# Optimization experiments

Measured on AMD Instinct MI355X. Metric: run time of the kernel, lower is better.

Reference implementation:

```python
import jax, jax.numpy as jnp
import numpy as np

N = 50000      # num_nodes
E = 800000     # num_edges (avg degree 16)
IC, OC = 2, 2  # in_channels, out_channels
DIN, DOUT = 128, 128
K = 3          # number of hops


def setup_inputs() -> dict:
    key = jax.random.key(0)
    k1, k2, k3, k4 = jax.random.split(key, 4)
    x = jax.random.normal(k1, (IC, N, DIN), dtype=jnp.float32)
    edge_index = jax.random.randint(k2, (2, E), 0, N, dtype=jnp.int32)
    a = np.sqrt(6.0 / (DIN + DOUT)).astype(np.float32)  # xavier_uniform bound
    W = jax.random.uniform(k3, (OC, IC, DIN, DOUT), minval=-a, maxval=a, dtype=jnp.float32)
    params = jax.random.uniform(k4, (OC, IC, K + 1), minval=0.0, maxval=0.01, dtype=jnp.float32)
    return {"x": x, "edge_index": edge_index, "W": W, "params": params}


def reference(x, edge_index, W, params):
    # x: [IC, N, DIN]; edge_index: [2, E]; W: [OC, IC, DIN, DOUT]; params: [OC, IC, K+1]
    n = x.shape[1]
    k_hops = params.shape[-1] - 1
    row, col = edge_index[0], edge_index[1]

    # normalize_adj: symmetric D^-1/2 A D^-1/2 on unit-valued edges
    deg = jax.ops.segment_sum(jnp.ones(row.shape[0], x.dtype), row, num_segments=n)
    dinv = jnp.where(deg > 0, jax.lax.rsqrt(deg), jnp.zeros_like(deg))
    val = dinv[row] * dinv[col]  # [E]

    def spmm(X):  # A_norm @ X per channel; X: [IC, N, d]
        gathered = X[:, col, :] * val[None, :, None]  # [IC, E, d]
        return jax.vmap(lambda g: jax.ops.segment_sum(g, row, num_segments=n))(gathered)

    # Hop features: H[m] = A^m x, computed once (hoisting the redundant spmm in the torch loop)
    hops = [x]
    for _ in range(k_hops):
        hops.append(spmm(hops[-1]))
    H = jnp.stack(hops)  # [K+1, IC, N, DIN]

    # out[i] = sum_j sum_m params[i,j,m] * (A^m x_j) @ W[i,j]
    return jnp.einsum('mjnd,ijm,ijdf->inf', H, params, W)  # [OC, N, DOUT]
```

## Files before the change

kernel.cpp:

```cpp
#include <hip/hip_runtime.h>
#include <hip/hip_bf16.h>
#include <stdint.h>

#define NN 50000
#define NE 800000
#define D 128
#define KH 3
#define SCAN_B ((NN + 255) / 256)

typedef __attribute__((ext_vector_type(8))) __bf16 bf16x8;
typedef __attribute__((ext_vector_type(4))) float f32x4;

__device__ __forceinline__ uint16_t bf16_rne(float f) {
  uint32_t u = __builtin_bit_cast(uint32_t, f);
  u = (u + 0x7fffu + ((u >> 16) & 1u)) >> 16;
  return (uint16_t)u;
}

#define GLDS16(gp, lp)                                                         \
  __builtin_amdgcn_global_load_lds(                                            \
      (__attribute__((address_space(1))) void*)(gp),                           \
      (__attribute__((address_space(3))) void*)(lp), 16, 0, 0)

__global__ void k_deg(const int* __restrict__ row, int* __restrict__ deg) {
  int e = blockIdx.x * 256 + threadIdx.x;
  if (e < NE) atomicAdd(&deg[row[e]], 1);
}

__global__ void k_dinv_bsum(const int* __restrict__ deg, float* __restrict__ dinv,
                            int* __restrict__ bsum) {
  __shared__ int s[256];
  int t = threadIdx.x;
  int i = blockIdx.x * 256 + t;
  int d = (i < NN) ? deg[i] : 0;
  if (i < NN) dinv[i] = (d > 0) ? rsqrtf((float)d) : 0.0f;
  s[t] = d;
  __syncthreads();
  for (int off = 128; off > 0; off >>= 1) {
    if (t < off) s[t] += s[t + off];
    __syncthreads();
  }
  if (t == 0) bsum[blockIdx.x] = s[0];
}

__global__ void k_bscan(const int* __restrict__ bsum, int* __restrict__ boff) {
  __shared__ int s[256];
  int t = threadIdx.x;
  int v = (t < SCAN_B) ? bsum[t] : 0;
  s[t] = v;
  __syncthreads();
  for (int off = 1; off < 256; off <<= 1) {
    int u = (t >= off) ? s[t - off] : 0;
    __syncthreads();
    s[t] += u;
    __syncthreads();
  }
  boff[t] = s[t] - v;
}

__global__ void k_rpwrite(const int* __restrict__ deg, const int* __restrict__ boff,
                          int* __restrict__ rp, int* __restrict__ cur) {
  __shared__ int s[256];
  int t = threadIdx.x;
  int i = blockIdx.x * 256 + t;
  int v = (i < NN) ? deg[i] : 0;
  s[t] = v;
  __syncthreads();
  for (int off = 1; off < 256; off <<= 1) {
    int u = (t >= off) ? s[t - off] : 0;
    __syncthreads();
    s[t] += u;
    __syncthreads();
  }
  if (i < NN) {
    int r = boff[blockIdx.x] + s[t] - v;
    rp[i] = r;
    cur[i] = r;
  }
  if (i == 0) rp[NN] = NE;
}

__global__ void k_scatter(const int* __restrict__ row, const int* __restrict__ col,
                          const float* __restrict__ dinv, int* __restrict__ cur,
                          int2* __restrict__ csr) {
  int e = blockIdx.x * 256 + threadIdx.x;
  if (e < NE) {
    int r = row[e], c = col[e];
    int pos = atomicAdd(&cur[r], 1);
    csr[pos] = make_int2(c, __float_as_int(dinv[r] * dinv[c]));
  }
}

__global__ void k_prep_c(const float* __restrict__ x, const float* __restrict__ W,
                         const float* __restrict__ params, uint16_t* __restrict__ dst,
                         uint16_t* __restrict__ wb) {
  int b = blockIdx.x, t = threadIdx.x;
  if (b < NN) {
    int idx = b * 256 + t;
    int n = idx >> 8, c = idx & 255, j = c >> 7, dd = c & 127;
    dst[idx] = bf16_rne(x[(size_t)j * NN * D + (size_t)n * D + dd]);
  } else {
    int idx = (b - NN) * 256 + t;
    int c = idx >> 10, k = idx & 1023;
    int i = c >> 7, f = c & 127, m = k >> 8, j = (k >> 7) & 1, dd = k & 127;
    float p = params[(i * 2 + j) * 4 + m];
    float w = W[((i * 2 + j) * 128 + dd) * 128 + f];
    wb[idx] = bf16_rne(p * w);
  }
}

__global__ void k_wbig_f(const float* __restrict__ W, const float* __restrict__ params,
                         uint16_t* __restrict__ wb) {
  int idx = blockIdx.x * 256 + threadIdx.x;
  if (idx >= 2 * 256 * 512) return;
  int j = idx >> 17, c = (idx >> 9) & 255, k = idx & 511;
  int i = c >> 7, f = c & 127, m = k >> 7, dd = k & 127;
  float p = params[(i * 2 + j) * 4 + m];
  float w = W[((i * 2 + j) * 128 + dd) * 128 + f];
  wb[idx] = bf16_rne(p * w);
}

__global__ void k_x2h_f(const float* __restrict__ xj, uint16_t* __restrict__ dst) {
  int idx = blockIdx.x * 256 + threadIdx.x;
  if (idx < NN * D) dst[idx] = bf16_rne(xj[idx]);
}

template <int NCH>
__global__ void k_spmm(const int* __restrict__ rp, const int2* __restrict__ csr,
                       const uint16_t* __restrict__ src, uint16_t* __restrict__ dst) {
  constexpr int STRIDE = NCH * 128;
  typedef uint32_t gvec __attribute__((ext_vector_type(NCH)));
  const int lane = threadIdx.x & 63;
  const int wid = threadIdx.x >> 6;
  const int r = blockIdx.x * 4 + wid;
  if (r >= NN) return;
  const int s = __builtin_amdgcn_readfirstlane(rp[r]);
  const int e = __builtin_amdgcn_readfirstlane(rp[r + 1]);
  const int lo = lane * 2 * NCH;

  float a[2 * NCH] = {};
  int i = s;
  for (; i + 8 <= e; i += 8) {
    int2 cv[8];
    gvec g[8];
#pragma unroll
    for (int u = 0; u < 8; ++u) cv[u] = csr[i + u];
#pragma unroll
    for (int u = 0; u < 8; ++u)
      g[u] = *(const gvec*)(src + (size_t)cv[u].x * STRIDE + lo);
#pragma unroll
    for (int u = 0; u < 8; ++u) {
      float v = __int_as_float(cv[u].y);
#pragma unroll
      for (int q = 0; q < NCH; ++q) {
        a[2 * q] = fmaf(v, __builtin_bit_cast(float, g[u][q] << 16), a[2 * q]);
        a[2 * q + 1] =
            fmaf(v, __builtin_bit_cast(float, g[u][q] & 0xffff0000u), a[2 * q + 1]);
      }
    }
  }
  for (; i + 4 <= e; i += 4) {
    int2 cv[4];
    gvec g[4];
#pragma unroll
    for (int u = 0; u < 4; ++u) cv[u] = csr[i + u];
#pragma unroll
    for (int u = 0; u < 4; ++u)
      g[u] = *(const gvec*)(src + (size_t)cv[u].x * STRIDE + lo);
#pragma unroll
    for (int u = 0; u < 4; ++u) {
      float v = __int_as_float(cv[u].y);
#pragma unroll
      for (int q = 0; q < NCH; ++q) {
        a[2 * q] = fmaf(v, __builtin_bit_cast(float, g[u][q] << 16), a[2 * q]);
        a[2 * q + 1] =
            fmaf(v, __builtin_bit_cast(float, g[u][q] & 0xffff0000u), a[2 * q + 1]);
      }
    }
  }
  for (; i < e; ++i) {
    int2 cv = csr[i];
    float v = __int_as_float(cv.y);
    gvec g = *(const gvec*)(src + (size_t)cv.x * STRIDE + lo);
#pragma unroll
    for (int q = 0; q < NCH; ++q) {
      a[2 * q] = fmaf(v, __builtin_bit_cast(float, g[q] << 16), a[2 * q]);
      a[2 * q + 1] = fmaf(v, __builtin_bit_cast(float, g[q] & 0xffff0000u), a[2 * q + 1]);
    }
  }
  gvec o;
#pragma unroll
  for (int q = 0; q < NCH; ++q)
    o[q] = ((uint32_t)bf16_rne(a[2 * q + 1]) << 16) | (uint32_t)bf16_rne(a[2 * q]);
  *(gvec*)(dst + (size_t)r * STRIDE + lo) = o;
}

template <int KTOT, int HOPW, int ACCUM>
__global__ __launch_bounds__(256) void k_gemm(
    const uint16_t* __restrict__ h0, const uint16_t* __restrict__ h1,
    const uint16_t* __restrict__ h2, const uint16_t* __restrict__ h3,
    const uint16_t* __restrict__ wb, float* __restrict__ out) {
  __shared__ __align__(16) uint16_t As[128 * 32];
  __shared__ __align__(16) uint16_t Bs[128 * 32];
  const uint16_t* hops[4] = {h0, h1, h2, h3};
  int t = threadIdx.x;
  int lane = t & 63, wid = t >> 6;
  int wm = wid >> 1, wn = wid & 1;
  int m0 = blockIdx.x * 128;
  int c0 = blockIdx.y * 128;
  int rl = lane & 15, q = lane >> 4;
  f32x4 acc[4][4] = {};
#pragma unroll
  for (int hop = 0; hop < KTOT / HOPW; ++hop) {
    const uint16_t* hm = hops[hop];
    for (int kin = 0; kin < HOPW; kin += 32) {
      int k0 = hop * HOPW + kin;
#pragma unroll
      for (int rr = 0; rr < 2; ++rr) {
        int c = rr * 256 + t;
        int row = c >> 2, kcL = c & 3;
        int kcG = kcL ^ (row & 3);
        int gr = m0 + row;
        gr = gr < NN ? gr : NN - 1;
        GLDS16(hm + (size_t)gr * HOPW + kin + kcG * 8, &As[c * 8]);
      }
#pragma unroll
      for (int rr = 0; rr < 2; ++rr) {
        int c = rr * 256 + t;
        int cc = c >> 2, kcL = c & 3;
        int kcG = kcL ^ (cc & 3);
        GLDS16(wb + (size_t)(c0 + cc) * KTOT + k0 + kcG * 8, &Bs[c * 8]);
      }
      __syncthreads();
      bf16x8 af[4], bq[4];
#pragma unroll
      for (int f = 0; f < 4; ++f) {
        int row = wm * 64 + f * 16 + rl;
        int kc = q ^ (rl & 3);
        af[f] = *(const bf16x8*)(&As[row * 32 + kc * 8]);
      }
#pragma unroll
      for (int f = 0; f < 4; ++f) {
        int row = wn * 64 + f * 16 + rl;
        int kc = q ^ (rl & 3);
        bq[f] = *(const bf16x8*)(&Bs[row * 32 + kc * 8]);
      }
#pragma unroll
      for (int fm = 0; fm < 4; ++fm)
#pragma unroll
        for (int fn = 0; fn < 4; ++fn)
          acc[fm][fn] = __builtin_amdgcn_mfma_f32_16x16x32_bf16(af[fm], bq[fn],
                                                                acc[fm][fn], 0, 0, 0);
      __syncthreads();
    }
  }
  int iOut = blockIdx.y;
#pragma unroll
  for (int fm = 0; fm < 4; ++fm) {
#pragma unroll
    for (int r = 0; r < 4; ++r) {
      int rowg = m0 + wm * 64 + fm * 16 + q * 4 + r;
      if (rowg >= NN) continue;
      float* op = out + ((size_t)iOut * NN + rowg) * D;
#pragma unroll
      for (int fn = 0; fn < 4; ++fn) {
        int colg = wn * 64 + fn * 16 + rl;
        if (ACCUM)
          op[colg] += acc[fm][fn][r];
        else
          op[colg] = acc[fm][fn][r];
      }
    }
  }
}

extern "C" void kernel_launch(void* const* d_in, const int* in_sizes, int n_in,
                              void* d_out, int out_size, void* d_ws, size_t ws_size,
                              hipStream_t stream) {
  (void)in_sizes; (void)n_in; (void)out_size;
  const float* x = (const float*)d_in[0];
  const int* ei = (const int*)d_in[1];
  const float* W = (const float*)d_in[2];
  const float* params = (const float*)d_in[3];
  float* out = (float*)d_out;
  char* ws = (char*)d_ws;

  size_t off = 0;
  auto take = [&](size_t bytes) {
    char* p = ws + off;
    off = (off + bytes + 255) & ~(size_t)255;
    return p;
  };
  int* deg = (int*)take((size_t)NN * 4);
  float* dinv = (float*)take((size_t)NN * 4);
  int* rp = (int*)take((size_t)(NN + 1) * 4);
  int* cur = (int*)take((size_t)NN * 4);
  int* bsum = (int*)take(256 * 4);
  int* boff = (int*)take(256 * 4);
  int2* csr = (int2*)take((size_t)NE * 8);
  uint16_t* wb = (uint16_t*)take((size_t)256 * 1024 * 2);
  size_t fixed = off;

  hipMemsetAsync(deg, 0, (size_t)NN * 4, stream);
  k_deg<<<(NE + 255) / 256, 256, 0, stream>>>(ei, deg);
  k_dinv_bsum<<<SCAN_B, 256, 0, stream>>>(deg, dinv, bsum);
  k_bscan<<<1, 256, 0, stream>>>(bsum, boff);
  k_rpwrite<<<SCAN_B, 256, 0, stream>>>(deg, boff, rp, cur);
  k_scatter<<<(NE + 255) / 256, 256, 0, stream>>>(ei, ei + NE, dinv, cur, csr);

  size_t hopC = (size_t)NN * 256 * 2;
  size_t needC = fixed + 4 * hopC + 1024;

  if (ws_size >= needC) {
    uint16_t* hop[4];
    for (int m = 0; m < 4; ++m) hop[m] = (uint16_t*)take(hopC);
    k_prep_c<<<NN + 1024, 256, 0, stream>>>(x, W, params, hop[0], wb);
    for (int m = 1; m <= KH; ++m)
      k_spmm<2><<<(NN + 3) / 4, 256, 0, stream>>>(rp, csr, hop[m - 1], hop[m]);
    dim3 grid((NN + 127) / 128, 2);
    k_gemm<1024, 256, 0><<<grid, 256, 0, stream>>>(hop[0], hop[1], hop[2], hop[3],
                                                   wb, out);
  } else {
    size_t hopF = (size_t)NN * 128 * 2;
    uint16_t* hop[4];
    for (int m = 0; m < 4; ++m) hop[m] = (uint16_t*)take(hopF);
    k_wbig_f<<<(2 * 256 * 512 + 255) / 256, 256, 0, stream>>>(W, params, wb);
    for (int j = 0; j < 2; ++j) {
      k_x2h_f<<<(NN * D + 255) / 256, 256, 0, stream>>>(x + (size_t)j * NN * D, hop[0]);
      for (int m = 1; m <= KH; ++m)
        k_spmm<1><<<(NN + 3) / 4, 256, 0, stream>>>(rp, csr, hop[m - 1], hop[m]);
      dim3 grid((NN + 127) / 128, 2);
      if (j == 0)
        k_gemm<512, 128, 0><<<grid, 256, 0, stream>>>(hop[0], hop[1], hop[2], hop[3],
                                                      wb, out);
      else
        k_gemm<512, 128, 1><<<grid, 256, 0, stream>>>(hop[0], hop[1], hop[2], hop[3],
                                                      wb + 256 * 512, out);
    }
  }
}
```

Before: 417.0 us.

## Fuse block scan into rpwrite, vectorize prep, split-wave SpMM, K=64 GEMM tiles

Removes the separate block-offset scan kernel by having each rpwrite block reduce the preceding block sums itself. Vectorizes the x-to-bf16 conversion to 8 elements per thread. Restructures SpMM so each half-wave handles alternate edges with wider 16-byte gathers, then combines the halves with a cross-lane shuffle. Doubles the GEMM K tile to 64 with an 8-way XOR swizzle, which halves the number of barriers but doubles LDS use per block.

```diff
diff --git a/kernel.cpp b/kernel.cpp
--- a/kernel.cpp
+++ b/kernel.cpp
@@ -15,6 +15,9 @@
   uint32_t u = __builtin_bit_cast(uint32_t, f);
   u = (u + 0x7fffu + ((u >> 16) & 1u)) >> 16;
   return (uint16_t)u;
+}
+__device__ __forceinline__ uint32_t bf16_pack(float lo, float hi) {
+  return ((uint32_t)bf16_rne(hi) << 16) | (uint32_t)bf16_rne(lo);
 }
 
 #define GLDS16(gp, lp)                                                         \
@@ -43,26 +46,22 @@
   if (t == 0) bsum[blockIdx.x] = s[0];
 }
 
-__global__ void k_bscan(const int* __restrict__ bsum, int* __restrict__ boff) {
-  __shared__ int s[256];
-  int t = threadIdx.x;
-  int v = (t < SCAN_B) ? bsum[t] : 0;
-  s[t] = v;
-  __syncthreads();
-  for (int off = 1; off < 256; off <<= 1) {
-    int u = (t >= off) ? s[t - off] : 0;
-    __syncthreads();
-    s[t] += u;
-    __syncthreads();
-  }
-  boff[t] = s[t] - v;
-}
-
-__global__ void k_rpwrite(const int* __restrict__ deg, const int* __restrict__ boff,
+__global__ void k_rpwrite(const int* __restrict__ deg, const int* __restrict__ bsum,
                           int* __restrict__ rp, int* __restrict__ cur) {
   __shared__ int s[256];
+  __shared__ int sboff;
   int t = threadIdx.x;
-  int i = blockIdx.x * 256 + t;
+  int b = blockIdx.x;
+  int pv = (t < b) ? bsum[t] : 0;
+  s[t] = pv;
+  __syncthreads();
+  for (int off = 128; off > 0; off >>= 1) {
+    if (t < off) s[t] += s[t + off];
+    __syncthreads();
+  }
+  if (t == 0) sboff = s[0];
+  __syncthreads();
+  int i = b * 256 + t;
   int v = (i < NN) ? deg[i] : 0;
   s[t] = v;
   __syncthreads();
@@ -73,7 +72,7 @@
     __syncthreads();
   }
   if (i < NN) {
-    int r = boff[blockIdx.x] + s[t] - v;
+    int r = sboff + s[t] - v;
     rp[i] = r;
     cur[i] = r;
   }
@@ -91,16 +90,26 @@
   }
 }
 
+#define XB 6250
 __global__ void k_prep_c(const float* __restrict__ x, const float* __restrict__ W,
                          const float* __restrict__ params, uint16_t* __restrict__ dst,
                          uint16_t* __restrict__ wb) {
   int b = blockIdx.x, t = threadIdx.x;
-  if (b < NN) {
-    int idx = b * 256 + t;
-    int n = idx >> 8, c = idx & 255, j = c >> 7, dd = c & 127;
-    dst[idx] = bf16_rne(x[(size_t)j * NN * D + (size_t)n * D + dd]);
+  if (b < XB) {
+    int base = (b * 256 + t) * 8;
+    int n = base >> 8, c0 = base & 255;
+    int j = c0 >> 7, dd = c0 & 127;
+    const float* xp = x + (size_t)j * NN * D + (size_t)n * D + dd;
+    float4 f0 = *(const float4*)xp;
+    float4 f1 = *(const float4*)(xp + 4);
+    uint4 o;
+    o.x = bf16_pack(f0.x, f0.y);
+    o.y = bf16_pack(f0.z, f0.w);
+    o.z = bf16_pack(f1.x, f1.y);
+    o.w = bf16_pack(f1.z, f1.w);
+    *(uint4*)(dst + base) = o;
   } else {
-    int idx = (b - NN) * 256 + t;
+    int idx = (b - XB) * 256 + t;
     int c = idx >> 10, k = idx & 1023;
     int i = c >> 7, f = c & 127, m = k >> 8, j = (k >> 7) & 1, dd = k & 127;
     float p = params[(i * 2 + j) * 4 + m];
@@ -129,22 +138,24 @@
 __global__ void k_spmm(const int* __restrict__ rp, const int2* __restrict__ csr,
                        const uint16_t* __restrict__ src, uint16_t* __restrict__ dst) {
   constexpr int STRIDE = NCH * 128;
-  typedef uint32_t gvec __attribute__((ext_vector_type(NCH)));
+  constexpr int NDW = NCH * 2;
+  typedef uint32_t gvec __attribute__((ext_vector_type(NDW)));
   const int lane = threadIdx.x & 63;
   const int wid = threadIdx.x >> 6;
   const int r = blockIdx.x * 4 + wid;
   if (r >= NN) return;
   const int s = __builtin_amdgcn_readfirstlane(rp[r]);
   const int e = __builtin_amdgcn_readfirstlane(rp[r + 1]);
-  const int lo = lane * 2 * NCH;
-
-  float a[2 * NCH] = {};
+  const int half = lane >> 5;
+  const int lo = (lane & 31) * 2 * NDW;
+
+  float a[2 * NDW] = {};
   int i = s;
-  for (; i + 8 <= e; i += 8) {
+  for (; i + 16 <= e; i += 16) {
     int2 cv[8];
     gvec g[8];
 #pragma unroll
-    for (int u = 0; u < 8; ++u) cv[u] = csr[i + u];
+    for (int u = 0; u < 8; ++u) cv[u] = csr[i + 2 * u + half];
 #pragma unroll
     for (int u = 0; u < 8; ++u)
       g[u] = *(const gvec*)(src + (size_t)cv[u].x * STRIDE + lo);
@@ -152,47 +163,41 @@
     for (int u = 0; u < 8; ++u) {
       float v = __int_as_float(cv[u].y);
 #pragma unroll
-      for (int q = 0; q < NCH; ++q) {
+      for (int q = 0; q < NDW; ++q) {
         a[2 * q] = fmaf(v, __builtin_bit_cast(float, g[u][q] << 16), a[2 * q]);
         a[2 * q + 1] =
             fmaf(v, __builtin_bit_cast(float, g[u][q] & 0xffff0000u), a[2 * q + 1]);
       }
     }
   }
-  for (; i + 4 <= e; i += 4) {
-    int2 cv[4];
-    gvec g[4];
-#pragma unroll
-    for (int u = 0; u < 4; ++u) cv[u] = csr[i + u];
-#pragma unroll
-    for (int u = 0; u < 4; ++u)
-      g[u] = *(const gvec*)(src + (size_t)cv[u].x * STRIDE + lo);
-#pragma unroll
-    for (int u = 0; u < 4; ++u) {
-      float v = __int_as_float(cv[u].y);
-#pragma unroll
-      for (int q = 0; q < NCH; ++q) {
-        a[2 * q] = fmaf(v, __builtin_bit_cast(float, g[u][q] << 16), a[2 * q]);
-        a[2 * q + 1] =
-            fmaf(v, __builtin_bit_cast(float, g[u][q] & 0xffff0000u), a[2 * q + 1]);
-      }
-    }
-  }
-  for (; i < e; ++i) {
+  for (; i + 2 <= e; i += 2) {
+    int2 cv = csr[i + half];
+    float v = __int_as_float(cv.y);
+    gvec g = *(const gvec*)(src + (size_t)cv.x * STRIDE + lo);
+#pragma unroll
+    for (int q = 0; q < NDW; ++q) {
+      a[2 * q] = fmaf(v, __builtin_bit_cast(float, g[q] << 16), a[2 * q]);
+      a[2 * q + 1] = fmaf(v, __builtin_bit_cast(float, g[q] & 0xffff0000u), a[2 * q + 1]);
+    }
+  }
+  if (i < e && half == 0) {
     int2 cv = csr[i];
     float v = __int_as_float(cv.y);
     gvec g = *(const gvec*)(src + (size_t)cv.x * STRIDE + lo);
 #pragma unroll
-    for (int q = 0; q < NCH; ++q) {
+    for (int q = 0; q < NDW; ++q) {
       a[2 * q] = fmaf(v, __builtin_bit_cast(float, g[q] << 16), a[2 * q]);
       a[2 * q + 1] = fmaf(v, __builtin_bit_cast(float, g[q] & 0xffff0000u), a[2 * q + 1]);
     }
   }
-  gvec o;
-#pragma unroll
-  for (int q = 0; q < NCH; ++q)
-    o[q] = ((uint32_t)bf16_rne(a[2 * q + 1]) << 16) | (uint32_t)bf16_rne(a[2 * q]);
-  *(gvec*)(dst + (size_t)r * STRIDE + lo) = o;
+#pragma unroll
+  for (int q = 0; q < 2 * NDW; ++q) a[q] += __shfl_xor(a[q], 32);
+  if (half == 0) {
+    gvec o;
+#pragma unroll
+    for (int q = 0; q < NDW; ++q) o[q] = bf16_pack(a[2 * q], a[2 * q + 1]);
+    *(gvec*)(dst + (size_t)r * STRIDE + lo) = o;
+  }
 }
 
 template <int KTOT, int HOPW, int ACCUM>
@@ -200,8 +205,8 @@
     const uint16_t* __restrict__ h0, const uint16_t* __restrict__ h1,
     const uint16_t* __restrict__ h2, const uint16_t* __restrict__ h3,
     const uint16_t* __restrict__ wb, float* __restrict__ out) {
-  __shared__ __align__(16) uint16_t As[128 * 32];
-  __shared__ __align__(16) uint16_t Bs[128 * 32];
+  __shared__ __align__(16) uint16_t As[128 * 64];
+  __shared__ __align__(16) uint16_t Bs[128 * 64];
   const uint16_t* hops[4] = {h0, h1, h2, h3};
   int t = threadIdx.x;
   int lane = t & 63, wid = t >> 6;
@@ -213,44 +218,44 @@
 #pragma unroll
   for (int hop = 0; hop < KTOT / HOPW; ++hop) {
     const uint16_t* hm = hops[hop];
-    for (int kin = 0; kin < HOPW; kin += 32) {
+#pragma unroll
+    for (int kin = 0; kin < HOPW; kin += 64) {
       int k0 = hop * HOPW + kin;
 #pragma unroll
-      for (int rr = 0; rr < 2; ++rr) {
+      for (int rr = 0; rr < 4; ++rr) {
         int c = rr * 256 + t;
-        int row = c >> 2, kcL = c & 3;
-        int kcG = kcL ^ (row & 3);
+        int row = c >> 3, kcL = c & 7;
+        int kcG = kcL ^ (row & 7);
         int gr = m0 + row;
         gr = gr < NN ? gr : NN - 1;
         GLDS16(hm + (size_t)gr * HOPW + kin + kcG * 8, &As[c * 8]);
       }
 #pragma unroll
-      for (int rr = 0; rr < 2; ++rr) {
+      for (int rr = 0; rr < 4; ++rr) {
         int c = rr * 256 + t;
-        int cc = c >> 2, kcL = c & 3;
-        int kcG = kcL ^ (cc & 3);
+        int cc = c >> 3, kcL = c & 7;
+        int kcG = kcL ^ (cc & 7);
         GLDS16(wb + (size_t)(c0 + cc) * KTOT + k0 + kcG * 8, &Bs[c * 8]);
       }
       __syncthreads();
-      bf16x8 af[4], bq[4];
-#pragma unroll
-      for (int f = 0; f < 4; ++f) {
-        int row = wm * 64 + f * 16 + rl;
-        int kc = q ^ (rl & 3);
-        af[f] = *(const bf16x8*)(&As[row * 32 + kc * 8]);
-      }
-#pragma unroll
-      for (int f = 0; f < 4; ++f) {
-        int row = wn * 64 + f * 16 + rl;
-        int kc = q ^ (rl & 3);
-        bq[f] = *(const bf16x8*)(&Bs[row * 32 + kc * 8]);
-      }
-#pragma unroll
-      for (int fm = 0; fm < 4; ++fm)
-#pragma unroll
-        for (int fn = 0; fn < 4; ++fn)
-          acc[fm][fn] = __builtin_amdgcn_mfma_f32_16x16x32_bf16(af[fm], bq[fn],
-                                                                acc[fm][fn], 0, 0, 0);
+#pragma unroll
+      for (int kq2 = 0; kq2 < 2; ++kq2) {
+        int w = kq2 * 4 + q;
+        bf16x8 af[4], bq[4];
+#pragma unroll
+        for (int f = 0; f < 4; ++f) {
+          int row = wm * 64 + f * 16 + rl;
+          af[f] = *(const bf16x8*)(&As[row * 64 + (w ^ (row & 7)) * 8]);
+          int col = wn * 64 + f * 16 + rl;
+          bq[f] = *(const bf16x8*)(&Bs[col * 64 + (w ^ (col & 7)) * 8]);
+        }
+#pragma unroll
+        for (int fm = 0; fm < 4; ++fm)
+#pragma unroll
+          for (int fn = 0; fn < 4; ++fn)
+            acc[fm][fn] = __builtin_amdgcn_mfma_f32_16x16x32_bf16(af[fm], bq[fn],
+                                                                  acc[fm][fn], 0, 0, 0);
+      }
       __syncthreads();
     }
   }
@@ -296,7 +301,6 @@
   int* rp = (int*)take((size_t)(NN + 1) * 4);
   int* cur = (int*)take((size_t)NN * 4);
   int* bsum = (int*)take(256 * 4);
-  int* boff = (int*)take(256 * 4);
   int2* csr = (int2*)take((size_t)NE * 8);
   uint16_t* wb = (uint16_t*)take((size_t)256 * 1024 * 2);
   size_t fixed = off;
@@ -304,8 +308,7 @@
   hipMemsetAsync(deg, 0, (size_t)NN * 4, stream);
   k_deg<<<(NE + 255) / 256, 256, 0, stream>>>(ei, deg);
   k_dinv_bsum<<<SCAN_B, 256, 0, stream>>>(deg, dinv, bsum);
-  k_bscan<<<1, 256, 0, stream>>>(bsum, boff);
-  k_rpwrite<<<SCAN_B, 256, 0, stream>>>(deg, boff, rp, cur);
+  k_rpwrite<<<SCAN_B, 256, 0, stream>>>(deg, bsum, rp, cur);
   k_scatter<<<(NE + 255) / 256, 256, 0, stream>>>(ei, ei + NE, dinv, cur, csr);
 
   size_t hopC = (size_t)NN * 256 * 2;
@@ -314,7 +317,7 @@
   if (ws_size >= needC) {
     uint16_t* hop[4];
     for (int m = 0; m < 4; ++m) hop[m] = (uint16_t*)take(hopC);
-    k_prep_c<<<NN + 1024, 256, 0, stream>>>(x, W, params, hop[0], wb);
+    k_prep_c<<<XB + 1024, 256, 0, stream>>>(x, W, params, hop[0], wb);
     for (int m = 1; m <= KH; ++m)
       k_spmm<2><<<(NN + 3) / 4, 256, 0, stream>>>(rp, csr, hop[m - 1], hop[m]);
     dim3 grid((NN + 127) / 128, 2);
```

New measurement: 411.1 us. Within noise of the previous version (-1.4%).
